# Kernel optimization log

Hardware: AMD Instinct MI355X
Metric: run time of the kernel (lower is better)

## Reference

```python
import jax, jax.numpy as jnp
import numpy as np

B, N, DIN, D, L = 16, 256, 32, 64, 3  # batch, nodes, input feat, emb_dim, num_layer


def setup_inputs() -> dict:
    key = jax.random.key(0)
    ks = jax.random.split(key, 8)
    fea = jax.random.normal(ks[0], (B, N, DIN), jnp.float32)
    # binary dense adjacency (float, as the repo differentiates through it)
    adj = (jax.random.uniform(ks[1], (B, N, N)) < 0.125).astype(jnp.float32)

    def g(k, shape, scale=0.05):
        return jax.random.normal(k, shape, jnp.float32) * scale

    return dict(
        fea=fea, adj=adj,
        enc_W=g(ks[2], (DIN, D)), enc_b=jnp.zeros((D,), jnp.float32),
        bond_W=g(ks[3], (L, D)),            # Linear(1, D, bias=False) per layer
        eps=jnp.zeros((L,), jnp.float32),   # GIN eps per layer
        W1=g(ks[4], (L, D, 2 * D)), b1=jnp.zeros((L, 2 * D), jnp.float32),
        g1=jnp.ones((L, 2 * D), jnp.float32), be1=jnp.zeros((L, 2 * D), jnp.float32),
        W2=g(ks[5], (L, 2 * D, D)), b2=jnp.zeros((L, D), jnp.float32),
        gbn=jnp.ones((L, D), jnp.float32), bbn=jnp.zeros((L, D), jnp.float32),
    )


def _bn(x, gamma, beta, eps=1e-5):
    # BatchNorm1d in training mode: per-channel stats over (batch, nodes)
    m = x.mean((0, 1), keepdims=True)
    v = x.var((0, 1), keepdims=True)
    return (x - m) * jax.lax.rsqrt(v + eps) * gamma + beta


def reference(fea, adj, enc_W, enc_b, bond_W, eps, W1, b1, g1, be1, W2, b2, gbn, bbn):
    x = fea @ enc_W + enc_b                      # [B,N,D] atom_encoder
    adj_ones = jnp.where(adj > 1.0, 1.0, adj)    # clamp multi-bonds to 1
    for l in range(L):
        # GINConv: dense propagate -> message relu(x_j + edge_attr) -> sum over neighbors
        edge = adj[..., None] * bond_W[l]                    # bond_encoder: [B,N,N,D]
        x_j = adj_ones[..., None] * x[:, None, :, :]         # [B,N,N,D] broadcast gather
        agg = jax.nn.relu(x_j + edge).sum(-2)                # [B,N,D] sum-reduce
        h = (1.0 + eps[l]) * x + agg
        # mlp: Linear(D,2D) -> BN -> ReLU -> Linear(2D,D)
        h = _bn(h @ W1[l] + b1[l], g1[l], be1[l])
        h = jax.nn.relu(h) @ W2[l] + b2[l]
        # outer batch norm; ReLU except last layer (drop_ratio=0 -> dropout no-op)
        h = _bn(h, gbn[l], bbn[l])
        x = h if l == L - 1 else jax.nn.relu(h)
    return x  # JK='last'
```

## Files before the change

kernel.cpp:

```cpp
#include <hip/hip_runtime.h>

#define NN 256
#define DIN 32
#define DD 64
#define D2 128
#define RTOT 4096
#define GBD 256
#define RPB 16
#define GBC 512
#define RPC 8
#define AST 32

typedef float f32x4 __attribute__((ext_vector_type(4)));
typedef float f32x2 __attribute__((ext_vector_type(2)));

__device__ __forceinline__ void fma4(f32x4& o, float s, const f32x4 w) {
  o[0] = fmaf(s, w[0], o[0]); o[1] = fmaf(s, w[1], o[1]);
  o[2] = fmaf(s, w[2], o[2]); o[3] = fmaf(s, w[3], o[3]);
}

__device__ __forceinline__ unsigned f2b(float f) {
  unsigned u = __float_as_uint(f);
  return (u + 0x7FFFu + ((u >> 16) & 1u)) >> 16;
}
__device__ __forceinline__ float b2f(unsigned short h) {
  return __uint_as_float(((unsigned)h) << 16);
}

__global__ __launch_bounds__(256) void enc_kernel(
    const float* __restrict__ fea, const float* __restrict__ W,
    const float* __restrict__ bias, float* __restrict__ x,
    float* __restrict__ accz) {
  if (blockIdx.x < 48) {
#pragma unroll
    for (int i = 0; i < 4; ++i)
      accz[blockIdx.x * 1024 + i * 256 + threadIdx.x] = 0.f;
  }
  int g = blockIdx.x * 256 + threadIdx.x;
  int r = g >> 6, c = g & 63;
  const float* fr = fea + r * DIN;
  float acc = bias[c];
#pragma unroll
  for (int k = 0; k < DIN; ++k) acc = fmaf(fr[k], W[k * DD + c], acc);
  x[g] = acc;
}

__global__ __launch_bounds__(256, 4) void bc_kernel(
    const float* __restrict__ adj, const float* __restrict__ x,
    const float* __restrict__ bondW, const float* __restrict__ epsp,
    const float* __restrict__ W1, const float* __restrict__ b1,
    const float* __restrict__ gbnp, const float* __restrict__ bbnp,
    const float* __restrict__ acc2p,
    int apply_bn,
    float* __restrict__ h1, float* __restrict__ acc1) {
  __shared__ unsigned short sYb[NN * DD];
  __shared__ float sh[RPC * DD];
  __shared__ float sSB[2 * DD];
  float* pst = (float*)sYb;
  const int tid = threadIdx.x, bid = blockIdx.x;
  const int lane = tid & 63, wv = tid >> 6;
  const int b = bid >> 5;
  const int r0 = (bid & 31) * RPC;

  if (apply_bn && tid < DD) {
    float s = acc2p[tid * AST], q = acc2p[(64 + tid) * AST];
    float mean = s * (1.f / RTOT);
    float var = fmaf(-mean, mean, q * (1.f / RTOT));
    float sc = gbnp[tid] * rsqrtf(var + 1e-5f);
    sSB[tid] = sc;
    sSB[64 + tid] = fmaf(-mean, sc, bbnp[tid]);
  }
  __syncthreads();

  const float* xb = x + (size_t)b * NN * DD;

  float a[2][4];
#pragma unroll
  for (int rr = 0; rr < 2; ++rr) {
    const float* adjr = adj + ((size_t)b * NN + r0 + wv * 2 + rr) * NN + lane;
#pragma unroll
    for (int ck = 0; ck < 4; ++ck) a[rr][ck] = adjr[ck * 64];
  }
  float xo[2];
#pragma unroll
  for (int rr = 0; rr < 2; ++rr)
    xo[rr] = xb[(size_t)(r0 + wv * 2 + rr) * DD + lane];
  f32x4 yv[16];
  {
    const f32x4* xb4 = (const f32x4*)xb;
#pragma unroll
    for (int k = 0; k < 16; ++k) yv[k] = xb4[tid + k * 256];
  }

  unsigned long long m[2][4];
#pragma unroll
  for (int rr = 0; rr < 2; ++rr)
#pragma unroll
    for (int ck = 0; ck < 4; ++ck) m[rr][ck] = __ballot(a[rr][ck] != 0.f);

  {
    const int d0 = (tid & 15) * 4;
    f32x4 bw4 = *(const f32x4*)&bondW[d0];
    f32x4 aS = {0, 0, 0, 0}, aB = {0, 0, 0, 0};
    if (apply_bn) { aS = *(const f32x4*)&sSB[d0]; aB = *(const f32x4*)&sSB[64 + d0]; }
    uint2* sy2 = (uint2*)sYb;
#pragma unroll
    for (int k = 0; k < 16; ++k) {
      f32x4 v = yv[k];
#pragma unroll
      for (int e = 0; e < 4; ++e) {
        float t = v[e];
        if (apply_bn) t = fmaxf(fmaf(t, aS[e], aB[e]), 0.f);
        v[e] = fmaxf(t + bw4[e], 0.f);
      }
      uint2 pk;
      pk.x = f2b(v[0]) | (f2b(v[1]) << 16);
      pk.y = f2b(v[2]) | (f2b(v[3]) << 16);
      sy2[tid + k * 256] = pk;
    }
  }
  __syncthreads();

  {
    float S = 0.f, Bv = 0.f;
    if (apply_bn) { S = sSB[lane]; Bv = sSB[64 + lane]; }
    float epv = 1.f + epsp[0];
#pragma unroll
    for (int rr = 0; rr < 2; ++rr) {
      float av = 0.f;
#pragma unroll
      for (int ck = 0; ck < 4; ++ck) {
        unsigned long long mm = m[rr][ck];
        const unsigned short* yb = sYb + ck * 64 * DD + lane;
        while (mm) {
          unsigned short v[8]; bool hb[8];
#pragma unroll
          for (int u = 0; u < 8; ++u) {
            bool ok = mm != 0ull;
            int j = ok ? (int)__builtin_ctzll(mm) : 0;
            mm &= mm - 1;
            hb[u] = ok;
            v[u] = yb[j * DD];
          }
#pragma unroll
          for (int u = 0; u < 8; ++u) av += hb[u] ? b2f(v[u]) : 0.f;
        }
      }
      float xv = xo[rr];
      if (apply_bn) xv = fmaxf(fmaf(xv, S, Bv), 0.f);
      sh[(wv * 2 + rr) * DD + lane] = fmaf(epv, xv, av);
    }
  }
  __syncthreads();

  {
    int row = tid >> 5, c0 = (tid & 31) * 4;
    f32x4 o = *(const f32x4*)&b1[c0];
#pragma unroll 4
    for (int d = 0; d < DD; d += 4) {
      f32x4 hv = *(const f32x4*)&sh[row * DD + d];
      f32x4 w0 = *(const f32x4*)&W1[(d + 0) * D2 + c0];
      f32x4 w1 = *(const f32x4*)&W1[(d + 1) * D2 + c0];
      f32x4 w2 = *(const f32x4*)&W1[(d + 2) * D2 + c0];
      f32x4 w3 = *(const f32x4*)&W1[(d + 3) * D2 + c0];
      fma4(o, hv[0], w0); fma4(o, hv[1], w1); fma4(o, hv[2], w2); fma4(o, hv[3], w3);
    }
    *(f32x4*)&h1[(size_t)(b * NN + r0 + row) * D2 + c0] = o;
    *(f32x4*)&pst[row * D2 + c0] = o;
    *(f32x4*)&pst[RPC * D2 + row * D2 + c0] = o * o;
  }
  __syncthreads();
  if (tid < D2) {
    float s = 0.f, q = 0.f;
#pragma unroll
    for (int g = 0; g < RPC; ++g) {
      s += pst[g * D2 + tid];
      q += pst[RPC * D2 + g * D2 + tid];
    }
    atomicAdd(acc1 + tid * AST, s);
    atomicAdd(acc1 + (128 + tid) * AST, q);
  }
}

__global__ __launch_bounds__(256) void d_kernel(
    const float* __restrict__ h1, const float* __restrict__ W2,
    const float* __restrict__ b2, const float* __restrict__ g1,
    const float* __restrict__ be1, float* __restrict__ h2,
    const float* __restrict__ acc1,
    float* __restrict__ acc2) {
  __shared__ float sW2[D2 * DD];
  __shared__ float sh1[RPB][D2 + 4];
  __shared__ float sS[D2], sB[D2];
  __shared__ float pst[2 * 8 * DD];
  int tid = threadIdx.x, bid = blockIdx.x;

  {
    const f32x4* w4 = (const f32x4*)W2;
    f32x4* s4 = (f32x4*)sW2;
#pragma unroll
    for (int i = 0; i < 8; ++i) s4[tid + i * 256] = w4[tid + i * 256];
  }
  if (tid < D2) {
    float mean = acc1[tid * AST] * (1.f / RTOT);
    float var = fmaf(-mean, mean, acc1[(128 + tid) * AST] * (1.f / RTOT));
    float sc = g1[tid] * rsqrtf(var + 1e-5f);
    sS[tid] = sc;
    sB[tid] = fmaf(-mean, sc, be1[tid]);
  }
  __syncthreads();
  {
    const f32x4* h14 = (const f32x4*)(h1 + (size_t)bid * RPB * D2);
#pragma unroll
    for (int ii = 0; ii < 2; ++ii) {
      int i = tid + ii * 256;
      f32x4 v = h14[i];
      int lr = i >> 5, c = (i & 31) * 4;
      v[0] = fmaxf(fmaf(v[0], sS[c + 0], sB[c + 0]), 0.f);
      v[1] = fmaxf(fmaf(v[1], sS[c + 1], sB[c + 1]), 0.f);
      v[2] = fmaxf(fmaf(v[2], sS[c + 2], sB[c + 2]), 0.f);
      v[3] = fmaxf(fmaf(v[3], sS[c + 3], sB[c + 3]), 0.f);
      *(f32x4*)&sh1[lr][c] = v;
    }
  }
  __syncthreads();

  float* pssum = pst;
  float* pssq  = pst + 8 * DD;
  if (tid < 128) {
    int rg = tid >> 4;
    int c0 = (tid & 15) * 4;
    f32x4 bv = *(const f32x4*)&b2[c0];
    f32x4 o0 = bv, o1 = bv;
    for (int c = 0; c < D2; c += 4) {
      f32x4 s0 = *(const f32x4*)&sh1[rg * 2 + 0][c];
      f32x4 s1 = *(const f32x4*)&sh1[rg * 2 + 1][c];
      f32x4 w0 = *(const f32x4*)&sW2[(c + 0) * DD + c0];
      f32x4 w1 = *(const f32x4*)&sW2[(c + 1) * DD + c0];
      f32x4 w2 = *(const f32x4*)&sW2[(c + 2) * DD + c0];
      f32x4 w3 = *(const f32x4*)&sW2[(c + 3) * DD + c0];
      fma4(o0, s0[0], w0); fma4(o0, s0[1], w1); fma4(o0, s0[2], w2); fma4(o0, s0[3], w3);
      fma4(o1, s1[0], w0); fma4(o1, s1[1], w1); fma4(o1, s1[2], w2); fma4(o1, s1[3], w3);
    }
    size_t gr = (size_t)(bid * RPB + rg * 2) * DD + c0;
    *(f32x4*)&h2[gr] = o0;
    *(f32x4*)&h2[gr + DD] = o1;
    *(f32x4*)&pssum[rg * DD + c0] = o0 + o1;
    *(f32x4*)&pssq[rg * DD + c0] = o0 * o0 + o1 * o1;
  }
  __syncthreads();
  if (tid < DD) {
    float s = 0.f, q = 0.f;
#pragma unroll
    for (int g = 0; g < 8; ++g) { s += pssum[g * DD + tid]; q += pssq[g * DD + tid]; }
    atomicAdd(acc2 + tid * AST, s);
    atomicAdd(acc2 + (64 + tid) * AST, q);
  }
}

__global__ __launch_bounds__(256) void fin_kernel(
    const float* __restrict__ h2, const float* __restrict__ gbn,
    const float* __restrict__ bbn, const float* __restrict__ acc2,
    float* __restrict__ outp) {
  __shared__ float sS2[DD], sB2[DD];
  int tid = threadIdx.x, bid = blockIdx.x;
  if (tid < 64) {
    float mean = acc2[tid * AST] * (1.f / RTOT);
    float var = fmaf(-mean, mean, acc2[(64 + tid) * AST] * (1.f / RTOT));
    float sc = gbn[tid] * rsqrtf(var + 1e-5f);
    sS2[tid] = sc;
    sB2[tid] = fmaf(-mean, sc, bbn[tid]);
  }
  __syncthreads();
#pragma unroll
  for (int k = 0; k < 4; ++k) {
    int idx = bid * 1024 + k * 256 + tid;
    int c = idx & 63;
    outp[idx] = fmaf(h2[idx], sS2[c], sB2[c]);
  }
}

extern "C" void kernel_launch(void* const* d_in, const int* in_sizes, int n_in,
                              void* d_out, int out_size, void* d_ws, size_t ws_size,
                              hipStream_t stream) {
  const float* fea  = (const float*)d_in[0];
  const float* adj  = (const float*)d_in[1];
  const float* encW = (const float*)d_in[2];
  const float* encb = (const float*)d_in[3];
  const float* bondW= (const float*)d_in[4];
  const float* eps  = (const float*)d_in[5];
  const float* W1   = (const float*)d_in[6];
  const float* b1   = (const float*)d_in[7];
  const float* g1   = (const float*)d_in[8];
  const float* be1  = (const float*)d_in[9];
  const float* W2   = (const float*)d_in[10];
  const float* b2   = (const float*)d_in[11];
  const float* gbn  = (const float*)d_in[12];
  const float* bbn  = (const float*)d_in[13];
  float* out = (float*)d_out;
  float* ws  = (float*)d_ws;

  float* x   = ws;
  float* h1  = ws + 262144;
  float* acc = ws + 786432;

  enc_kernel<<<1024, 256, 0, stream>>>(fea, encW, encb, x, acc);
  for (int l = 0; l < 3; ++l) {
    float* accl = acc + (size_t)l * 512 * AST;
    bc_kernel<<<GBC, 256, 0, stream>>>(
        adj, x, bondW + l * DD, eps + l, W1 + l * DD * D2, b1 + l * D2,
        l ? gbn + (l - 1) * DD : gbn, l ? bbn + (l - 1) * DD : bbn,
        l ? acc + (size_t)(l - 1) * 512 * AST + 256 * AST : acc, l > 0 ? 1 : 0,
        h1, accl);
    d_kernel<<<GBD, 256, 0, stream>>>(h1, W2 + l * D2 * DD, b2 + l * DD,
                                      g1 + l * D2, be1 + l * D2, x,
                                      accl, accl + 256 * AST);
  }
  fin_kernel<<<256, 256, 0, stream>>>(x, gbn + 2 * DD, bbn + 2 * DD,
                                      acc + (size_t)2 * 512 * AST + 256 * AST, out);
}
```

Baseline: 87.53 us.

## Use 512-thread blocks in bc_kernel and halve rows per block in d_kernel

```diff
diff --git a/kernel.cpp b/kernel.cpp
--- a/kernel.cpp
+++ b/kernel.cpp
@@ -5,8 +5,8 @@
 #define DD 64
 #define D2 128
 #define RTOT 4096
-#define GBD 256
-#define RPB 16
+#define GBD 512
+#define RPB 8
 #define GBC 512
 #define RPC 8
 #define AST 32
@@ -45,7 +45,7 @@
   x[g] = acc;
 }
 
-__global__ __launch_bounds__(256, 4) void bc_kernel(
+__global__ __launch_bounds__(512, 4) void bc_kernel(
     const float* __restrict__ adj, const float* __restrict__ x,
     const float* __restrict__ bondW, const float* __restrict__ epsp,
     const float* __restrict__ W1, const float* __restrict__ b1,
@@ -74,100 +74,90 @@
 
   const float* xb = x + (size_t)b * NN * DD;
 
-  float a[2][4];
-#pragma unroll
-  for (int rr = 0; rr < 2; ++rr) {
-    const float* adjr = adj + ((size_t)b * NN + r0 + wv * 2 + rr) * NN + lane;
-#pragma unroll
-    for (int ck = 0; ck < 4; ++ck) a[rr][ck] = adjr[ck * 64];
-  }
-  float xo[2];
-#pragma unroll
-  for (int rr = 0; rr < 2; ++rr)
-    xo[rr] = xb[(size_t)(r0 + wv * 2 + rr) * DD + lane];
-  f32x4 yv[16];
+  float a4[4];
+  {
+    const float* adjr = adj + ((size_t)b * NN + r0 + wv) * NN + lane;
+#pragma unroll
+    for (int ck = 0; ck < 4; ++ck) a4[ck] = adjr[ck * 64];
+  }
+  float xo = xb[(size_t)(r0 + wv) * DD + lane];
+  f32x4 yv[8];
   {
     const f32x4* xb4 = (const f32x4*)xb;
 #pragma unroll
-    for (int k = 0; k < 16; ++k) yv[k] = xb4[tid + k * 256];
-  }
-
-  unsigned long long m[2][4];
-#pragma unroll
-  for (int rr = 0; rr < 2; ++rr)
-#pragma unroll
-    for (int ck = 0; ck < 4; ++ck) m[rr][ck] = __ballot(a[rr][ck] != 0.f);
-
-  {
-    const int d0 = (tid & 15) * 4;
-    f32x4 bw4 = *(const f32x4*)&bondW[d0];
-    f32x4 aS = {0, 0, 0, 0}, aB = {0, 0, 0, 0};
-    if (apply_bn) { aS = *(const f32x4*)&sSB[d0]; aB = *(const f32x4*)&sSB[64 + d0]; }
+    for (int k = 0; k < 8; ++k) yv[k] = xb4[tid + k * 512];
+  }
+
+  unsigned long long m[4];
+#pragma unroll
+  for (int ck = 0; ck < 4; ++ck) m[ck] = __ballot(a4[ck] != 0.f);
+
+  {
     uint2* sy2 = (uint2*)sYb;
 #pragma unroll
-    for (int k = 0; k < 16; ++k) {
+    for (int k = 0; k < 8; ++k) {
+      int i = tid + k * 512;
+      int d0 = (i & 15) * 4;
       f32x4 v = yv[k];
 #pragma unroll
       for (int e = 0; e < 4; ++e) {
         float t = v[e];
-        if (apply_bn) t = fmaxf(fmaf(t, aS[e], aB[e]), 0.f);
-        v[e] = fmaxf(t + bw4[e], 0.f);
+        if (apply_bn) t = fmaxf(fmaf(t, sSB[d0 + e], sSB[64 + d0 + e]), 0.f);
+        v[e] = fmaxf(t + bondW[d0 + e], 0.f);
       }
       uint2 pk;
       pk.x = f2b(v[0]) | (f2b(v[1]) << 16);
       pk.y = f2b(v[2]) | (f2b(v[3]) << 16);
-      sy2[tid + k * 256] = pk;
-    }
-  }
-  __syncthreads();
-
-  {
-    float S = 0.f, Bv = 0.f;
-    if (apply_bn) { S = sSB[lane]; Bv = sSB[64 + lane]; }
-    float epv = 1.f + epsp[0];
-#pragma unroll
-    for (int rr = 0; rr < 2; ++rr) {
-      float av = 0.f;
-#pragma unroll
-      for (int ck = 0; ck < 4; ++ck) {
-        unsigned long long mm = m[rr][ck];
-        const unsigned short* yb = sYb + ck * 64 * DD + lane;
-        while (mm) {
-          unsigned short v[8]; bool hb[8];
-#pragma unroll
-          for (int u = 0; u < 8; ++u) {
-            bool ok = mm != 0ull;
-            int j = ok ? (int)__builtin_ctzll(mm) : 0;
-            mm &= mm - 1;
-            hb[u] = ok;
-            v[u] = yb[j * DD];
-          }
-#pragma unroll
-          for (int u = 0; u < 8; ++u) av += hb[u] ? b2f(v[u]) : 0.f;
+      sy2[i] = pk;
+    }
+  }
+  __syncthreads();
+
+  {
+    float av = 0.f;
+#pragma unroll
+    for (int ck = 0; ck < 4; ++ck) {
+      unsigned long long mm = m[ck];
+      const unsigned short* yb = sYb + ck * 64 * DD + lane;
+      while (mm) {
+        unsigned short v[8]; bool hb[8];
+#pragma unroll
+        for (int u = 0; u < 8; ++u) {
+          bool ok = mm != 0ull;
+          int j = ok ? (int)__builtin_ctzll(mm) : 0;
+          mm &= mm - 1;
+          hb[u] = ok;
+          v[u] = yb[j * DD];
         }
+#pragma unroll
+        for (int u = 0; u < 8; ++u) av += hb[u] ? b2f(v[u]) : 0.f;
       }
-      float xv = xo[rr];
-      if (apply_bn) xv = fmaxf(fmaf(xv, S, Bv), 0.f);
-      sh[(wv * 2 + rr) * DD + lane] = fmaf(epv, xv, av);
-    }
-  }
-  __syncthreads();
-
-  {
-    int row = tid >> 5, c0 = (tid & 31) * 4;
-    f32x4 o = *(const f32x4*)&b1[c0];
+    }
+    float xv = xo;
+    if (apply_bn) xv = fmaxf(fmaf(xv, sSB[lane], sSB[64 + lane]), 0.f);
+    sh[wv * DD + lane] = fmaf(1.f + epsp[0], xv, av);
+  }
+  __syncthreads();
+
+  {
+    int row = tid >> 6, c0 = (tid & 63) * 2;
+    f32x2 o = *(const f32x2*)&b1[c0];
 #pragma unroll 4
     for (int d = 0; d < DD; d += 4) {
       f32x4 hv = *(const f32x4*)&sh[row * DD + d];
-      f32x4 w0 = *(const f32x4*)&W1[(d + 0) * D2 + c0];
-      f32x4 w1 = *(const f32x4*)&W1[(d + 1) * D2 + c0];
-      f32x4 w2 = *(const f32x4*)&W1[(d + 2) * D2 + c0];
-      f32x4 w3 = *(const f32x4*)&W1[(d + 3) * D2 + c0];
-      fma4(o, hv[0], w0); fma4(o, hv[1], w1); fma4(o, hv[2], w2); fma4(o, hv[3], w3);
-    }
-    *(f32x4*)&h1[(size_t)(b * NN + r0 + row) * D2 + c0] = o;
-    *(f32x4*)&pst[row * D2 + c0] = o;
-    *(f32x4*)&pst[RPC * D2 + row * D2 + c0] = o * o;
+      f32x2 w0 = *(const f32x2*)&W1[(d + 0) * D2 + c0];
+      f32x2 w1 = *(const f32x2*)&W1[(d + 1) * D2 + c0];
+      f32x2 w2 = *(const f32x2*)&W1[(d + 2) * D2 + c0];
+      f32x2 w3 = *(const f32x2*)&W1[(d + 3) * D2 + c0];
+      o[0] = fmaf(hv[0], w0[0], o[0]); o[1] = fmaf(hv[0], w0[1], o[1]);
+      o[0] = fmaf(hv[1], w1[0], o[0]); o[1] = fmaf(hv[1], w1[1], o[1]);
+      o[0] = fmaf(hv[2], w2[0], o[0]); o[1] = fmaf(hv[2], w2[1], o[1]);
+      o[0] = fmaf(hv[3], w3[0], o[0]); o[1] = fmaf(hv[3], w3[1], o[1]);
+    }
+    *(f32x2*)&h1[(size_t)(b * NN + r0 + row) * D2 + c0] = o;
+    *(f32x2*)&pst[row * D2 + c0] = o;
+    f32x2 oq; oq[0] = o[0] * o[0]; oq[1] = o[1] * o[1];
+    *(f32x2*)&pst[RPC * D2 + row * D2 + c0] = oq;
   }
   __syncthreads();
   if (tid < D2) {
@@ -191,7 +181,7 @@
   __shared__ float sW2[D2 * DD];
   __shared__ float sh1[RPB][D2 + 4];
   __shared__ float sS[D2], sB[D2];
-  __shared__ float pst[2 * 8 * DD];
+  __shared__ float pst[2 * RPB * DD];
   int tid = threadIdx.x, bid = blockIdx.x;
 
   {
@@ -209,49 +199,39 @@
   }
   __syncthreads();
   {
-    const f32x4* h14 = (const f32x4*)(h1 + (size_t)bid * RPB * D2);
-#pragma unroll
-    for (int ii = 0; ii < 2; ++ii) {
-      int i = tid + ii * 256;
-      f32x4 v = h14[i];
-      int lr = i >> 5, c = (i & 31) * 4;
-      v[0] = fmaxf(fmaf(v[0], sS[c + 0], sB[c + 0]), 0.f);
-      v[1] = fmaxf(fmaf(v[1], sS[c + 1], sB[c + 1]), 0.f);
-      v[2] = fmaxf(fmaf(v[2], sS[c + 2], sB[c + 2]), 0.f);
-      v[3] = fmaxf(fmaf(v[3], sS[c + 3], sB[c + 3]), 0.f);
-      *(f32x4*)&sh1[lr][c] = v;
-    }
-  }
-  __syncthreads();
-
-  float* pssum = pst;
-  float* pssq  = pst + 8 * DD;
-  if (tid < 128) {
-    int rg = tid >> 4;
-    int c0 = (tid & 15) * 4;
-    f32x4 bv = *(const f32x4*)&b2[c0];
-    f32x4 o0 = bv, o1 = bv;
-    for (int c = 0; c < D2; c += 4) {
-      f32x4 s0 = *(const f32x4*)&sh1[rg * 2 + 0][c];
-      f32x4 s1 = *(const f32x4*)&sh1[rg * 2 + 1][c];
-      f32x4 w0 = *(const f32x4*)&sW2[(c + 0) * DD + c0];
-      f32x4 w1 = *(const f32x4*)&sW2[(c + 1) * DD + c0];
-      f32x4 w2 = *(const f32x4*)&sW2[(c + 2) * DD + c0];
-      f32x4 w3 = *(const f32x4*)&sW2[(c + 3) * DD + c0];
-      fma4(o0, s0[0], w0); fma4(o0, s0[1], w1); fma4(o0, s0[2], w2); fma4(o0, s0[3], w3);
-      fma4(o1, s1[0], w0); fma4(o1, s1[1], w1); fma4(o1, s1[2], w2); fma4(o1, s1[3], w3);
-    }
-    size_t gr = (size_t)(bid * RPB + rg * 2) * DD + c0;
-    *(f32x4*)&h2[gr] = o0;
-    *(f32x4*)&h2[gr + DD] = o1;
-    *(f32x4*)&pssum[rg * DD + c0] = o0 + o1;
-    *(f32x4*)&pssq[rg * DD + c0] = o0 * o0 + o1 * o1;
+    f32x4 v = ((const f32x4*)(h1 + (size_t)bid * RPB * D2))[tid];
+    int lr = tid >> 5, c = (tid & 31) * 4;
+    v[0] = fmaxf(fmaf(v[0], sS[c + 0], sB[c + 0]), 0.f);
+    v[1] = fmaxf(fmaf(v[1], sS[c + 1], sB[c + 1]), 0.f);
+    v[2] = fmaxf(fmaf(v[2], sS[c + 2], sB[c + 2]), 0.f);
+    v[3] = fmaxf(fmaf(v[3], sS[c + 3], sB[c + 3]), 0.f);
+    *(f32x4*)&sh1[lr][c] = v;
+  }
+  __syncthreads();
+
+  {
+    int row = tid >> 5, c0 = (tid & 31) * 2;
+    f32x2 o = *(const f32x2*)&b2[c0];
+#pragma unroll 8
+    for (int c = 0; c < D2; ++c) {
+      float hv = sh1[row][c];
+      f32x2 w = *(const f32x2*)&sW2[c * DD + c0];
+      o[0] = fmaf(hv, w[0], o[0]);
+      o[1] = fmaf(hv, w[1], o[1]);
+    }
+    *(f32x2*)&h2[(size_t)(bid * RPB + row) * DD + c0] = o;
+    *(f32x2*)&pst[row * DD + c0] = o;
+    f32x2 oq; oq[0] = o[0] * o[0]; oq[1] = o[1] * o[1];
+    *(f32x2*)&pst[RPB * DD + row * DD + c0] = oq;
   }
   __syncthreads();
   if (tid < DD) {
     float s = 0.f, q = 0.f;
 #pragma unroll
-    for (int g = 0; g < 8; ++g) { s += pssum[g * DD + tid]; q += pssq[g * DD + tid]; }
+    for (int g = 0; g < RPB; ++g) {
+      s += pst[g * DD + tid];
+      q += pst[RPB * DD + g * DD + tid];
+    }
     atomicAdd(acc2 + tid * AST, s);
     atomicAdd(acc2 + (64 + tid) * AST, q);
   }
@@ -306,7 +286,7 @@
   enc_kernel<<<1024, 256, 0, stream>>>(fea, encW, encb, x, acc);
   for (int l = 0; l < 3; ++l) {
     float* accl = acc + (size_t)l * 512 * AST;
-    bc_kernel<<<GBC, 256, 0, stream>>>(
+    bc_kernel<<<GBC, 512, 0, stream>>>(
         adj, x, bondW + l * DD, eps + l, W1 + l * DD * D2, b1 + l * D2,
         l ? gbn + (l - 1) * DD : gbn, l ? bbn + (l - 1) * DD : bbn,
         l ? acc + (size_t)(l - 1) * 512 * AST + 256 * AST : acc, l > 0 ? 1 : 0,
```

Result: slower. 105.4 us (+20.4%).

## Store intermediate activations x and h1 as bf16 and swizzle block order

Applied to the files above, without the earlier changes.

```diff
diff --git a/kernel.cpp b/kernel.cpp
--- a/kernel.cpp
+++ b/kernel.cpp
@@ -29,7 +29,7 @@
 
 __global__ __launch_bounds__(256) void enc_kernel(
     const float* __restrict__ fea, const float* __restrict__ W,
-    const float* __restrict__ bias, float* __restrict__ x,
+    const float* __restrict__ bias, unsigned short* __restrict__ xb16,
     float* __restrict__ accz) {
   if (blockIdx.x < 48) {
 #pragma unroll
@@ -37,30 +37,35 @@
       accz[blockIdx.x * 1024 + i * 256 + threadIdx.x] = 0.f;
   }
   int g = blockIdx.x * 256 + threadIdx.x;
-  int r = g >> 6, c = g & 63;
+  int r = g >> 5, c0 = (g & 31) * 2;
   const float* fr = fea + r * DIN;
-  float acc = bias[c];
-#pragma unroll
-  for (int k = 0; k < DIN; ++k) acc = fmaf(fr[k], W[k * DD + c], acc);
-  x[g] = acc;
+  float a0 = bias[c0], a1 = bias[c0 + 1];
+#pragma unroll
+  for (int k = 0; k < DIN; ++k) {
+    float fv = fr[k];
+    a0 = fmaf(fv, W[k * DD + c0], a0);
+    a1 = fmaf(fv, W[k * DD + c0 + 1], a1);
+  }
+  ((unsigned*)xb16)[g] = f2b(a0) | (f2b(a1) << 16);
 }
 
 __global__ __launch_bounds__(256, 4) void bc_kernel(
-    const float* __restrict__ adj, const float* __restrict__ x,
+    const float* __restrict__ adj, const unsigned short* __restrict__ xb16,
     const float* __restrict__ bondW, const float* __restrict__ epsp,
     const float* __restrict__ W1, const float* __restrict__ b1,
     const float* __restrict__ gbnp, const float* __restrict__ bbnp,
     const float* __restrict__ acc2p,
     int apply_bn,
-    float* __restrict__ h1, float* __restrict__ acc1) {
+    unsigned short* __restrict__ h1b, float* __restrict__ acc1) {
   __shared__ unsigned short sYb[NN * DD];
   __shared__ float sh[RPC * DD];
   __shared__ float sSB[2 * DD];
   float* pst = (float*)sYb;
-  const int tid = threadIdx.x, bid = blockIdx.x;
+  const int tid = threadIdx.x;
+  const int sbid = ((blockIdx.x & 7) << 6) + (blockIdx.x >> 3);
   const int lane = tid & 63, wv = tid >> 6;
-  const int b = bid >> 5;
-  const int r0 = (bid & 31) * RPC;
+  const int b = sbid >> 5;
+  const int r0 = (sbid & 31) * RPC;
 
   if (apply_bn && tid < DD) {
     float s = acc2p[tid * AST], q = acc2p[(64 + tid) * AST];
@@ -72,7 +77,7 @@
   }
   __syncthreads();
 
-  const float* xb = x + (size_t)b * NN * DD;
+  const unsigned short* xb = xb16 + (size_t)b * NN * DD;
 
   float a[2][4];
 #pragma unroll
@@ -81,15 +86,15 @@
 #pragma unroll
     for (int ck = 0; ck < 4; ++ck) a[rr][ck] = adjr[ck * 64];
   }
-  float xo[2];
+  unsigned short xo[2];
 #pragma unroll
   for (int rr = 0; rr < 2; ++rr)
     xo[rr] = xb[(size_t)(r0 + wv * 2 + rr) * DD + lane];
-  f32x4 yv[16];
-  {
-    const f32x4* xb4 = (const f32x4*)xb;
-#pragma unroll
-    for (int k = 0; k < 16; ++k) yv[k] = xb4[tid + k * 256];
+  uint4 yv[8];
+  {
+    const uint4* xb4 = (const uint4*)xb;
+#pragma unroll
+    for (int k = 0; k < 8; ++k) yv[k] = xb4[tid + k * 256];
   }
 
   unsigned long long m[2][4];
@@ -99,24 +104,32 @@
     for (int ck = 0; ck < 4; ++ck) m[rr][ck] = __ballot(a[rr][ck] != 0.f);
 
   {
-    const int d0 = (tid & 15) * 4;
-    f32x4 bw4 = *(const f32x4*)&bondW[d0];
-    f32x4 aS = {0, 0, 0, 0}, aB = {0, 0, 0, 0};
-    if (apply_bn) { aS = *(const f32x4*)&sSB[d0]; aB = *(const f32x4*)&sSB[64 + d0]; }
-    uint2* sy2 = (uint2*)sYb;
-#pragma unroll
-    for (int k = 0; k < 16; ++k) {
-      f32x4 v = yv[k];
-#pragma unroll
-      for (int e = 0; e < 4; ++e) {
-        float t = v[e];
-        if (apply_bn) t = fmaxf(fmaf(t, aS[e], aB[e]), 0.f);
-        v[e] = fmaxf(t + bw4[e], 0.f);
+    const int d0 = (tid & 7) * 8;
+    float BW8[8], S8[8], B8[8];
+#pragma unroll
+    for (int j = 0; j < 8; ++j) {
+      BW8[j] = bondW[d0 + j];
+      S8[j] = apply_bn ? sSB[d0 + j] : 0.f;
+      B8[j] = apply_bn ? sSB[64 + d0 + j] : 0.f;
+    }
+    uint4* sy4 = (uint4*)sYb;
+#pragma unroll
+    for (int k = 0; k < 8; ++k) {
+      unsigned w[4] = {yv[k].x, yv[k].y, yv[k].z, yv[k].w};
+      unsigned o[4];
+#pragma unroll
+      for (int q = 0; q < 4; ++q) {
+        float f0 = __uint_as_float(w[q] << 16);
+        float f1 = __uint_as_float(w[q] & 0xFFFF0000u);
+        if (apply_bn) {
+          f0 = fmaxf(fmaf(f0, S8[2 * q], B8[2 * q]), 0.f);
+          f1 = fmaxf(fmaf(f1, S8[2 * q + 1], B8[2 * q + 1]), 0.f);
+        }
+        f0 = fmaxf(f0 + BW8[2 * q], 0.f);
+        f1 = fmaxf(f1 + BW8[2 * q + 1], 0.f);
+        o[q] = f2b(f0) | (f2b(f1) << 16);
       }
-      uint2 pk;
-      pk.x = f2b(v[0]) | (f2b(v[1]) << 16);
-      pk.y = f2b(v[2]) | (f2b(v[3]) << 16);
-      sy2[tid + k * 256] = pk;
+      sy4[tid + k * 256] = make_uint4(o[0], o[1], o[2], o[3]);
     }
   }
   __syncthreads();
@@ -146,7 +159,7 @@
           for (int u = 0; u < 8; ++u) av += hb[u] ? b2f(v[u]) : 0.f;
         }
       }
-      float xv = xo[rr];
+      float xv = b2f(xo[rr]);
       if (apply_bn) xv = fmaxf(fmaf(xv, S, Bv), 0.f);
       sh[(wv * 2 + rr) * DD + lane] = fmaf(epv, xv, av);
     }
@@ -165,7 +178,10 @@
       f32x4 w3 = *(const f32x4*)&W1[(d + 3) * D2 + c0];
       fma4(o, hv[0], w0); fma4(o, hv[1], w1); fma4(o, hv[2], w2); fma4(o, hv[3], w3);
     }
-    *(f32x4*)&h1[(size_t)(b * NN + r0 + row) * D2 + c0] = o;
+    uint2 hp;
+    hp.x = f2b(o[0]) | (f2b(o[1]) << 16);
+    hp.y = f2b(o[2]) | (f2b(o[3]) << 16);
+    *(uint2*)&h1b[(size_t)(b * NN + r0 + row) * D2 + c0] = hp;
     *(f32x4*)&pst[row * D2 + c0] = o;
     *(f32x4*)&pst[RPC * D2 + row * D2 + c0] = o * o;
   }
@@ -183,9 +199,9 @@
 }
 
 __global__ __launch_bounds__(256) void d_kernel(
-    const float* __restrict__ h1, const float* __restrict__ W2,
+    const unsigned short* __restrict__ h1b, const float* __restrict__ W2,
     const float* __restrict__ b2, const float* __restrict__ g1,
-    const float* __restrict__ be1, float* __restrict__ h2,
+    const float* __restrict__ be1, unsigned short* __restrict__ xb16,
     const float* __restrict__ acc1,
     float* __restrict__ acc2) {
   __shared__ float sW2[D2 * DD];
@@ -209,17 +225,16 @@
   }
   __syncthreads();
   {
-    const f32x4* h14 = (const f32x4*)(h1 + (size_t)bid * RPB * D2);
-#pragma unroll
-    for (int ii = 0; ii < 2; ++ii) {
-      int i = tid + ii * 256;
-      f32x4 v = h14[i];
-      int lr = i >> 5, c = (i & 31) * 4;
-      v[0] = fmaxf(fmaf(v[0], sS[c + 0], sB[c + 0]), 0.f);
-      v[1] = fmaxf(fmaf(v[1], sS[c + 1], sB[c + 1]), 0.f);
-      v[2] = fmaxf(fmaf(v[2], sS[c + 2], sB[c + 2]), 0.f);
-      v[3] = fmaxf(fmaf(v[3], sS[c + 3], sB[c + 3]), 0.f);
-      *(f32x4*)&sh1[lr][c] = v;
+    uint4 hv = ((const uint4*)(h1b + (size_t)bid * RPB * D2))[tid];
+    int row = tid >> 4, cb = (tid & 15) * 8;
+    unsigned w[4] = {hv.x, hv.y, hv.z, hv.w};
+#pragma unroll
+    for (int q = 0; q < 4; ++q) {
+      float f0 = __uint_as_float(w[q] << 16);
+      float f1 = __uint_as_float(w[q] & 0xFFFF0000u);
+      int c = cb + 2 * q;
+      sh1[row][c]     = fmaxf(fmaf(f0, sS[c],     sB[c]),     0.f);
+      sh1[row][c + 1] = fmaxf(fmaf(f1, sS[c + 1], sB[c + 1]), 0.f);
     }
   }
   __syncthreads();
@@ -242,8 +257,13 @@
       fma4(o1, s1[0], w0); fma4(o1, s1[1], w1); fma4(o1, s1[2], w2); fma4(o1, s1[3], w3);
     }
     size_t gr = (size_t)(bid * RPB + rg * 2) * DD + c0;
-    *(f32x4*)&h2[gr] = o0;
-    *(f32x4*)&h2[gr + DD] = o1;
+    uint2 p0, p1;
+    p0.x = f2b(o0[0]) | (f2b(o0[1]) << 16);
+    p0.y = f2b(o0[2]) | (f2b(o0[3]) << 16);
+    p1.x = f2b(o1[0]) | (f2b(o1[1]) << 16);
+    p1.y = f2b(o1[2]) | (f2b(o1[3]) << 16);
+    *(uint2*)&xb16[gr] = p0;
+    *(uint2*)&xb16[gr + DD] = p1;
     *(f32x4*)&pssum[rg * DD + c0] = o0 + o1;
     *(f32x4*)&pssq[rg * DD + c0] = o0 * o0 + o1 * o1;
   }
@@ -258,7 +278,7 @@
 }
 
 __global__ __launch_bounds__(256) void fin_kernel(
-    const float* __restrict__ h2, const float* __restrict__ gbn,
+    const unsigned short* __restrict__ xb16, const float* __restrict__ gbn,
     const float* __restrict__ bbn, const float* __restrict__ acc2,
     float* __restrict__ outp) {
   __shared__ float sS2[DD], sB2[DD];
@@ -271,11 +291,17 @@
     sB2[tid] = fmaf(-mean, sc, bbn[tid]);
   }
   __syncthreads();
-#pragma unroll
-  for (int k = 0; k < 4; ++k) {
-    int idx = bid * 1024 + k * 256 + tid;
-    int c = idx & 63;
-    outp[idx] = fmaf(h2[idx], sS2[c], sB2[c]);
+  {
+    int g = bid * 256 + tid;
+    uint2 v = ((const uint2*)xb16)[g];
+    int e0 = g * 4;
+    int c0 = e0 & 63;
+    f32x4 o;
+    o[0] = fmaf(__uint_as_float(v.x << 16),        sS2[c0],     sB2[c0]);
+    o[1] = fmaf(__uint_as_float(v.x & 0xFFFF0000u), sS2[c0 + 1], sB2[c0 + 1]);
+    o[2] = fmaf(__uint_as_float(v.y << 16),        sS2[c0 + 2], sB2[c0 + 2]);
+    o[3] = fmaf(__uint_as_float(v.y & 0xFFFF0000u), sS2[c0 + 3], sB2[c0 + 3]);
+    *(f32x4*)&outp[e0] = o;
   }
 }
 
@@ -299,22 +325,22 @@
   float* out = (float*)d_out;
   float* ws  = (float*)d_ws;
 
-  float* x   = ws;
-  float* h1  = ws + 262144;
-  float* acc = ws + 786432;
-
-  enc_kernel<<<1024, 256, 0, stream>>>(fea, encW, encb, x, acc);
+  unsigned short* xb16 = (unsigned short*)ws;
+  unsigned short* h1b  = (unsigned short*)(ws + 131072);
+  float* acc = ws + 131072 + 262144;
+
+  enc_kernel<<<512, 256, 0, stream>>>(fea, encW, encb, xb16, acc);
   for (int l = 0; l < 3; ++l) {
     float* accl = acc + (size_t)l * 512 * AST;
     bc_kernel<<<GBC, 256, 0, stream>>>(
-        adj, x, bondW + l * DD, eps + l, W1 + l * DD * D2, b1 + l * D2,
+        adj, xb16, bondW + l * DD, eps + l, W1 + l * DD * D2, b1 + l * D2,
         l ? gbn + (l - 1) * DD : gbn, l ? bbn + (l - 1) * DD : bbn,
-        l ? acc + (size_t)(l - 1) * 512 * AST + 256 * AST : acc, l > 0 ? 1 : 0,
-        h1, accl);
-    d_kernel<<<GBD, 256, 0, stream>>>(h1, W2 + l * D2 * DD, b2 + l * DD,
-                                      g1 + l * D2, be1 + l * D2, x,
+        l ? acc + (size_t)(l - 1) * 512 * AST + 256 * AST : acc,
+        l > 0 ? 1 : 0, h1b, accl);
+    d_kernel<<<GBD, 256, 0, stream>>>(h1b, W2 + l * D2 * DD, b2 + l * DD,
+                                      g1 + l * D2, be1 + l * D2, xb16,
                                       accl, accl + 256 * AST);
   }
-  fin_kernel<<<256, 256, 0, stream>>>(x, gbn + 2 * DD, bbn + 2 * DD,
+  fin_kernel<<<256, 256, 0, stream>>>(xb16, gbn + 2 * DD, bbn + 2 * DD,
                                       acc + (size_t)2 * 512 * AST + 256 * AST, out);
 }
```

Result: no change. 86.97 us (-0.6%).
